# Kernel tuning notes

Measured on AMD Instinct MI355X. Metric: run time of the kernel, lower is better.

Reference implementation:

```python
import jax, jax.numpy as jnp
import numpy as np

D_MODEL = 1024
MAX_BIRTHS = 4
BIRTH_THRESHOLD = 0.45


def setup_inputs() -> dict:
    key = jax.random.key(0)
    ks = jax.random.split(key, 5)
    B, Tu, Tm, D = 4, 4096, 2048, D_MODEL
    return {
        "o_micro": jax.random.normal(ks[0], (B, Tu, D), jnp.float32),
        "o_macro": jax.random.normal(ks[1], (B, Tm, D), jnp.float32),
        "r_emer_acc": jax.random.uniform(ks[2], (B, Tu, Tm), jnp.float32),
        "chunk_size": 128,
        # vesica_field: Linear(2D -> D, no bias); torch weight layout (D, 2D)
        "W_vesica": jax.random.normal(ks[3], (D, 2 * D), jnp.float32) * (1.0 / np.sqrt(2.0 * D)),
        # birth_gate: Linear(D -> 1)
        "w_gate": jax.random.normal(ks[4], (D,), jnp.float32) * (1.0 / np.sqrt(float(D))),
        "b_gate": jnp.zeros((), jnp.float32),
        "threshold_bias": jnp.zeros((), jnp.float32),
    }


def reference(o_micro, o_macro, r_emer_acc, chunk_size, W_vesica, w_gate, b_gate, threshold_bias):
    B, Tu, D = o_micro.shape
    # accumulated resonance per micro token: mean over macro dim -> (B, Tu)
    micro_res = r_emer_acc.mean(axis=-1)
    # adjacent-pair resonance -> (B, Tu-1)
    pair_res = (micro_res[:, :-1] + micro_res[:, 1:]) * 0.5
    threshold = BIRTH_THRESHOLD + jnp.tanh(threshold_bias) * 0.2
    above = pair_res > threshold
    pair_scores = pair_res * above.astype(pair_res.dtype)
    k = MAX_BIRTHS  # min(max_births, Tu-1); Tu >> max_births here
    topk_vals, topk_idx = jax.lax.top_k(pair_scores, k)  # (B, k)
    birth_mask = topk_vals > 0
    n_births = birth_mask.sum()
    # gather parent pairs -> (B, k, D) each
    left = jnp.take_along_axis(o_micro, topk_idx[..., None], axis=1)
    right = jnp.take_along_axis(o_micro, (topk_idx + 1)[..., None], axis=1)
    combined = jnp.concatenate([left, right], axis=-1)  # (B, k, 2D)
    child = jnp.einsum("bkf,df->bkd", combined, W_vesica)
    gate = jax.nn.sigmoid(jnp.einsum("bkd,d->bk", child, w_gate) + b_gate)
    child = child * gate[..., None] * birth_mask[..., None].astype(child.dtype)
    # compact born children to the front (stable), zeros pad the tail —
    # identical to the torch ragged stack+pad given fixed width k
    order = jnp.argsort(~birth_mask, axis=1, stable=True)  # (B, k)
    child = jnp.take_along_axis(child, order[..., None], axis=1)
    o_macro_expanded = jnp.concatenate([o_macro, child], axis=1)  # (B, Tm+k, D)
    return o_macro_expanded, n_births
```

## Files before the change

### kernel.cpp

```cpp
#include <hip/hip_runtime.h>
#include <math.h>

#define BATCH 4
#define TU 4096
#define TM 2048
#define DM 1024
#define FF 2048
#define KB 4
#define NROWS (BATCH*KB)
#define OUT_TM (TM+KB)

typedef float fv4 __attribute__((ext_vector_type(4)));

__global__ __launch_bounds__(256) void k_mean_copy_u(
    const float* __restrict__ r_emer, const float* __restrict__ o_macro,
    const float* __restrict__ W, const float* __restrict__ w_gate,
    float* __restrict__ micro_res, float* __restrict__ u,
    float* __restrict__ out)
{
    const int tid  = threadIdx.x;
    const int lane = tid & 63;
    const int wave = tid >> 6;

    if (blockIdx.x < 4096) {
        const int row = blockIdx.x * 4 + wave;
        const fv4* rp = (const fv4*)(r_emer + (size_t)row * FF);
        fv4 a[8];
        #pragma unroll
        for (int j = 0; j < 8; ++j)
            a[j] = __builtin_nontemporal_load(rp + lane + 64 * j);

        const fv4* src = (const fv4*)o_macro;
        fv4* dst = (fv4*)out;
        const int e0 = blockIdx.x * 256 + tid;
        #pragma unroll
        for (int it = 0; it < 2; ++it) {
            int e = e0 + it * (4096 * 256);
            int b = e >> 19;
            int q = e & ((1 << 19) - 1);
            fv4 v = __builtin_nontemporal_load(src + e);
            __builtin_nontemporal_store(v, dst + (size_t)b * (OUT_TM * DM / 4) + q);
        }

        float s = 0.0f;
        #pragma unroll
        for (int j = 0; j < 8; ++j) s += a[j].x + a[j].y + a[j].z + a[j].w;
        #pragma unroll
        for (int off = 32; off >= 1; off >>= 1)
            s += __shfl_down(s, off, 64);
        if (lane == 0) micro_res[row] = s * (1.0f / 2048.0f);
    } else {
        const int bid = blockIdx.x - 4096;
        const float4* W4 = (const float4*)W;
        const int col = bid * 64 + lane;
        float4 acc = make_float4(0.f, 0.f, 0.f, 0.f);
        const int d0 = wave * 256;
        for (int d = d0; d < d0 + 256; ++d) {
            float g = w_gate[d];
            float4 wv = W4[(size_t)d * 512 + col];
            acc.x += g * wv.x; acc.y += g * wv.y;
            acc.z += g * wv.z; acc.w += g * wv.w;
        }
        __shared__ float4 part[4][64];
        part[wave][lane] = acc;
        __syncthreads();
        if (tid < 64) {
            float4 s0 = part[0][tid], s1 = part[1][tid];
            float4 s2 = part[2][tid], s3 = part[3][tid];
            float4 r;
            r.x = s0.x + s1.x + s2.x + s3.x;
            r.y = s0.y + s1.y + s2.y + s3.y;
            r.z = s0.z + s1.z + s2.z + s3.z;
            r.w = s0.w + s1.w + s2.w + s3.w;
            ((float4*)u)[bid * 64 + tid] = r;
        }
    }
}

__global__ __launch_bounds__(256) void k_topk_gate(
    const float* __restrict__ micro_res, const float* __restrict__ threshold_bias,
    const float* __restrict__ u, const float* __restrict__ o_micro,
    const float* __restrict__ b_gate,
    int* __restrict__ topk_idx, float* __restrict__ scale,
    float* __restrict__ counts)
{
    __shared__ float res[TU];
    __shared__ float rv[256];
    __shared__ int   ri[256];
    __shared__ int   sel[KB];
    __shared__ float selv[KB];
    __shared__ float red[4];
    __shared__ float sc[KB];

    const int b = blockIdx.x, tid = threadIdx.x;
    const int lane = tid & 63, wave = tid >> 6;
    const float* mr = micro_res + b * TU;
    for (int i = tid; i < TU; i += 256) res[i] = mr[i];
    __syncthreads();

    const float thr = 0.45f + tanhf(threshold_bias[0]) * 0.2f;

    for (int p = 0; p < KB; ++p) {
        float bv = -1.0f; int bi = 0x7fffffff;
        for (int t = tid; t < TU - 1; t += 256) {
            bool skip = false;
            for (int q = 0; q < p; ++q) if (sel[q] == t) skip = true;
            if (skip) continue;
            float pr = (res[t] + res[t + 1]) * 0.5f;
            float scv = pr > thr ? pr : 0.0f;
            if (scv > bv || (scv == bv && t < bi)) { bv = scv; bi = t; }
        }
        rv[tid] = bv; ri[tid] = bi;
        __syncthreads();
        for (int s = 128; s >= 1; s >>= 1) {
            if (tid < s) {
                float ov = rv[tid + s]; int oi = ri[tid + s];
                if (ov > rv[tid] || (ov == rv[tid] && oi < ri[tid])) {
                    rv[tid] = ov; ri[tid] = oi;
                }
            }
            __syncthreads();
        }
        if (tid == 0) { sel[p] = ri[0]; selv[p] = rv[0]; }
        __syncthreads();
    }

    const int f0 = tid * 8;
    const float4* up = (const float4*)(u + f0);
    const float4 u0 = up[0], u1 = up[1];
    for (int k = 0; k < KB; ++k) {
        const int idx = sel[k];
        const float* srcrow;
        int fo;
        if (f0 < DM) { srcrow = o_micro + ((size_t)b * TU + idx) * DM;     fo = f0; }
        else         { srcrow = o_micro + ((size_t)b * TU + idx + 1) * DM; fo = f0 - DM; }
        const float4* cp = (const float4*)(srcrow + fo);
        float4 c0 = cp[0], c1 = cp[1];
        float dsum = c0.x * u0.x + c0.y * u0.y + c0.z * u0.z + c0.w * u0.w
                   + c1.x * u1.x + c1.y * u1.y + c1.z * u1.z + c1.w * u1.w;
        #pragma unroll
        for (int off = 32; off >= 1; off >>= 1)
            dsum += __shfl_down(dsum, off, 64);
        if (lane == 0) red[wave] = dsum;
        __syncthreads();
        if (tid == 0) {
            float tot = red[0] + red[1] + red[2] + red[3] + b_gate[0];
            float g = 1.0f / (1.0f + expf(-tot));
            float m = selv[k] > 0.0f ? 1.0f : 0.0f;
            sc[k] = g * m;
        }
        __syncthreads();
    }

    if (tid < KB) {
        topk_idx[b * KB + tid] = sel[tid];
        scale[b * KB + tid] = sc[tid];
    }
    if (tid == 0) {
        float c = 0.f;
        for (int k = 0; k < KB; ++k) c += (selv[k] > 0.0f) ? 1.0f : 0.0f;
        counts[b] = c;
    }
}

__global__ __launch_bounds__(256) void k_child_out(
    const float* __restrict__ o_micro, const float* __restrict__ W,
    const int* __restrict__ topk_idx, const float* __restrict__ scale,
    const float* __restrict__ counts, float* __restrict__ out)
{
    const int d   = blockIdx.x;
    const int tid = threadIdx.x;
    const int lane = tid & 63;
    const int wave = tid >> 6;
    const int f0  = tid * 8;

    __shared__ int   sidx[NROWS];
    __shared__ float ssc[NROWS];
    if (tid < NROWS) { sidx[tid] = topk_idx[tid]; ssc[tid] = scale[tid]; }
    __syncthreads();

    const float4* wp = (const float4*)(W + (size_t)d * FF + f0);
    const float4 w0 = wp[0], w1 = wp[1];

    float acc[NROWS];
    #pragma unroll
    for (int r = 0; r < NROWS; ++r) {
        const int bb  = r >> 2;
        const int idx = sidx[r];
        const float* srcrow;
        int fo;
        if (f0 < DM) { srcrow = o_micro + ((size_t)bb * TU + idx) * DM;     fo = f0; }
        else         { srcrow = o_micro + ((size_t)bb * TU + idx + 1) * DM; fo = f0 - DM; }
        const float4* cp = (const float4*)(srcrow + fo);
        float4 c0 = cp[0], c1 = cp[1];
        acc[r] = c0.x * w0.x + c0.y * w0.y + c0.z * w0.z + c0.w * w0.w
               + c1.x * w1.x + c1.y * w1.y + c1.z * w1.z + c1.w * w1.w;
    }

    #pragma unroll
    for (int r = 0; r < NROWS; ++r) {
        float v = acc[r];
        #pragma unroll
        for (int off = 32; off >= 1; off >>= 1)
            v += __shfl_down(v, off, 64);
        acc[r] = v;
    }
    __shared__ float part[4][NROWS];
    if (lane == 0) {
        #pragma unroll
        for (int r = 0; r < NROWS; ++r) part[wave][r] = acc[r];
    }
    __syncthreads();
    if (tid < NROWS) {
        float v = (part[0][tid] + part[1][tid] + part[2][tid] + part[3][tid]) * ssc[tid];
        out[((size_t)(tid >> 2) * OUT_TM + TM + (tid & 3)) * DM + d] = v;
    }
    if (blockIdx.x == 0 && tid == 0)
        out[(size_t)BATCH * OUT_TM * DM] =
            counts[0] + counts[1] + counts[2] + counts[3];
}

extern "C" void kernel_launch(void* const* d_in, const int* in_sizes, int n_in,
                              void* d_out, int out_size, void* d_ws, size_t ws_size,
                              hipStream_t stream) {
    const float* o_micro   = (const float*)d_in[0];
    const float* o_macro   = (const float*)d_in[1];
    const float* r_emer    = (const float*)d_in[2];
    const float* W_vesica  = (const float*)d_in[4];
    const float* w_gate    = (const float*)d_in[5];
    const float* b_gate    = (const float*)d_in[6];
    const float* thr_bias  = (const float*)d_in[7];
    float* out = (float*)d_out;

    float* wsf       = (float*)d_ws;
    float* micro_res = wsf;
    float* u         = wsf + 16384;
    int*   topk_idx  = (int*)(wsf + 18432);
    float* scale     = wsf + 18448;
    float* counts    = wsf + 18464;

    k_mean_copy_u<<<4104, 256, 0, stream>>>(r_emer, o_macro, W_vesica, w_gate,
                                            micro_res, u, out);
    k_topk_gate<<<BATCH, 256, 0, stream>>>(micro_res, thr_bias, u, o_micro,
                                           b_gate, topk_idx, scale, counts);
    k_child_out<<<DM, 256, 0, stream>>>(o_micro, W_vesica, topk_idx, scale,
                                        counts, out);
}
```

Measured before the change: 323.4 us.

## Replace iterative argmax top-k with single-pass packed-key top-4 merge reduction

The top-k kernel used four sequential argmax passes over all pairs, each with a full shared-memory tree reduction. It now packs score and inverted index into a 64-bit key, keeps a per-thread sorted top-4 list, and merges those lists in one tree reduction. The block grows to 1024 threads so each thread handles fewer elements. This is meant to cut the latency of a small serial kernel. Tie-breaking relies on the key encoding matching the stable lower-index order of the reference.

```diff
diff --git a/kernel.cpp b/kernel.cpp
--- a/kernel.cpp
+++ b/kernel.cpp
@@ -11,6 +11,7 @@
 #define OUT_TM (TM+KB)
 
 typedef float fv4 __attribute__((ext_vector_type(4)));
+typedef unsigned long long u64;
 
 __global__ __launch_bounds__(256) void k_mean_copy_u(
     const float* __restrict__ r_emer, const float* __restrict__ o_macro,
@@ -77,7 +78,7 @@
     }
 }
 
-__global__ __launch_bounds__(256) void k_topk_gate(
+__global__ __launch_bounds__(1024) void k_topk_gate(
     const float* __restrict__ micro_res, const float* __restrict__ threshold_bias,
     const float* __restrict__ u, const float* __restrict__ o_micro,
     const float* __restrict__ b_gate,
@@ -85,66 +86,82 @@
     float* __restrict__ counts)
 {
     __shared__ float res[TU];
-    __shared__ float rv[256];
-    __shared__ int   ri[256];
+    __shared__ u64   lst[1024][4];
     __shared__ int   sel[KB];
     __shared__ float selv[KB];
-    __shared__ float red[4];
+    __shared__ float red[16];
     __shared__ float sc[KB];
 
     const int b = blockIdx.x, tid = threadIdx.x;
     const int lane = tid & 63, wave = tid >> 6;
-    const float* mr = micro_res + b * TU;
-    for (int i = tid; i < TU; i += 256) res[i] = mr[i];
+
+    ((float4*)res)[tid] = ((const float4*)(micro_res + b * TU))[tid];
     __syncthreads();
 
     const float thr = 0.45f + tanhf(threshold_bias[0]) * 0.2f;
 
-    for (int p = 0; p < KB; ++p) {
-        float bv = -1.0f; int bi = 0x7fffffff;
-        for (int t = tid; t < TU - 1; t += 256) {
-            bool skip = false;
-            for (int q = 0; q < p; ++q) if (sel[q] == t) skip = true;
-            if (skip) continue;
-            float pr = (res[t] + res[t + 1]) * 0.5f;
-            float scv = pr > thr ? pr : 0.0f;
-            if (scv > bv || (scv == bv && t < bi)) { bv = scv; bi = t; }
-        }
-        rv[tid] = bv; ri[tid] = bi;
-        __syncthreads();
-        for (int s = 128; s >= 1; s >>= 1) {
-            if (tid < s) {
-                float ov = rv[tid + s]; int oi = ri[tid + s];
-                if (ov > rv[tid] || (ov == rv[tid] && oi < ri[tid])) {
-                    rv[tid] = ov; ri[tid] = oi;
-                }
+    u64 l[4] = {0ull, 0ull, 0ull, 0ull};
+    #pragma unroll
+    for (int j = 0; j < 4; ++j) {
+        int t = tid + j * 1024;
+        if (t >= TU - 1) continue;
+        float pr = (res[t] + res[t + 1]) * 0.5f;
+        float s  = pr > thr ? pr : 0.0f;
+        u64 key = ((u64)__float_as_uint(s) << 32) | (u64)(0xFFFFFFFFu - (unsigned)t);
+        if (key > l[3]) {
+            l[3] = key;
+            #pragma unroll
+            for (int i = 3; i > 0; --i)
+                if (l[i] > l[i - 1]) { u64 tmp = l[i]; l[i] = l[i - 1]; l[i - 1] = tmp; }
+        }
+    }
+    lst[tid][0] = l[0]; lst[tid][1] = l[1]; lst[tid][2] = l[2]; lst[tid][3] = l[3];
+    __syncthreads();
+
+    for (int s = 512; s >= 1; s >>= 1) {
+        if (tid < s) {
+            u64 a0 = lst[tid][0],   a1 = lst[tid][1],   a2 = lst[tid][2],   a3 = lst[tid][3];
+            u64 b0 = lst[tid+s][0], b1 = lst[tid+s][1], b2 = lst[tid+s][2], b3 = lst[tid+s][3];
+            u64 a[4] = {a0, a1, a2, a3};
+            u64 c[4] = {b0, b1, b2, b3};
+            u64 o[4]; int ia = 0, ib = 0;
+            #pragma unroll
+            for (int i = 0; i < 4; ++i) {
+                bool ta = (ib >= 4) || (ia < 4 && a[ia] >= c[ib]);
+                o[i] = ta ? a[ia] : c[ib];
+                ia += ta ? 1 : 0; ib += ta ? 0 : 1;
             }
-            __syncthreads();
-        }
-        if (tid == 0) { sel[p] = ri[0]; selv[p] = rv[0]; }
-        __syncthreads();
-    }
-
-    const int f0 = tid * 8;
-    const float4* up = (const float4*)(u + f0);
-    const float4 u0 = up[0], u1 = up[1];
+            lst[tid][0] = o[0]; lst[tid][1] = o[1]; lst[tid][2] = o[2]; lst[tid][3] = o[3];
+        }
+        __syncthreads();
+    }
+
+    if (tid < KB) {
+        u64 key = lst[0][tid];
+        sel[tid]  = (int)(0xFFFFFFFFu - (unsigned)(key & 0xFFFFFFFFu));
+        selv[tid] = __uint_as_float((unsigned)(key >> 32));
+    }
+    __syncthreads();
+
+    const float2 uv = ((const float2*)u)[tid];
+    const int f0 = tid * 2;
     for (int k = 0; k < KB; ++k) {
         const int idx = sel[k];
         const float* srcrow;
         int fo;
         if (f0 < DM) { srcrow = o_micro + ((size_t)b * TU + idx) * DM;     fo = f0; }
         else         { srcrow = o_micro + ((size_t)b * TU + idx + 1) * DM; fo = f0 - DM; }
-        const float4* cp = (const float4*)(srcrow + fo);
-        float4 c0 = cp[0], c1 = cp[1];
-        float dsum = c0.x * u0.x + c0.y * u0.y + c0.z * u0.z + c0.w * u0.w
-                   + c1.x * u1.x + c1.y * u1.y + c1.z * u1.z + c1.w * u1.w;
+        float2 c = *(const float2*)(srcrow + fo);
+        float dsum = c.x * uv.x + c.y * uv.y;
         #pragma unroll
         for (int off = 32; off >= 1; off >>= 1)
             dsum += __shfl_down(dsum, off, 64);
         if (lane == 0) red[wave] = dsum;
         __syncthreads();
         if (tid == 0) {
-            float tot = red[0] + red[1] + red[2] + red[3] + b_gate[0];
+            float tot = b_gate[0];
+            #pragma unroll
+            for (int w = 0; w < 16; ++w) tot += red[w];
             float g = 1.0f / (1.0f + expf(-tot));
             float m = selv[k] > 0.0f ? 1.0f : 0.0f;
             sc[k] = g * m;
@@ -241,8 +258,8 @@
 
     k_mean_copy_u<<<4104, 256, 0, stream>>>(r_emer, o_macro, W_vesica, w_gate,
                                             micro_res, u, out);
-    k_topk_gate<<<BATCH, 256, 0, stream>>>(micro_res, thr_bias, u, o_micro,
-                                           b_gate, topk_idx, scale, counts);
+    k_topk_gate<<<BATCH, 1024, 0, stream>>>(micro_res, thr_bias, u, o_micro,
+                                            b_gate, topk_idx, scale, counts);
     k_child_out<<<DM, 256, 0, stream>>>(o_micro, W_vesica, topk_idx, scale,
                                         counts, out);
 }
```

Measured after the change: 315.6 us. 1.02x faster.
